# Kernel optimization log

Measured on AMD Instinct MI355X. Metric: run time of the kernel, lower is better.

## Reference

```python
import jax, jax.numpy as jnp
import numpy as np

D_MODEL = 1024
D_FF = 4096
N_EXPERTS = 8
B, S = 4, 2048


def setup_inputs() -> dict:
    key = jax.random.key(0)
    ks = jax.random.split(key, 6)
    x = jax.random.normal(ks[0], (B, S, D_MODEL), dtype=jnp.float32)
    # router: nn.Linear(d_model, num_experts) with bias (default torch init ~ small)
    gate_W = jax.random.normal(ks[1], (N_EXPERTS, D_MODEL), dtype=jnp.float32) * 0.02
    gate_b = jnp.zeros((N_EXPERTS,), dtype=jnp.float32)
    # SwiGLU expert weights, bias-free; torch Linear stores [out, in]
    Wg = jax.random.normal(ks[2], (N_EXPERTS, D_FF, D_MODEL), dtype=jnp.float32) * 0.02
    W1 = jax.random.normal(ks[3], (N_EXPERTS, D_FF, D_MODEL), dtype=jnp.float32) * 0.02
    W2 = jax.random.normal(ks[4], (N_EXPERTS, D_MODEL, D_FF), dtype=jnp.float32) * (0.02 / np.sqrt(2.0))
    return {"x": x, "gate_W": gate_W, "gate_b": gate_b, "Wg": Wg, "W1": W1, "W2": W2,
            "num_experts_per_token": 2}


def reference(x, gate_W, gate_b, Wg, W1, W2, num_experts_per_token):
    """Eval-mode ExpertFeedForward: top-k gating + per-expert SwiGLU + weighted combine."""
    Bb, Ss, D = x.shape
    E = gate_W.shape[0]
    T = Bb * Ss
    xt = x.reshape(T, D)  # [T, D] tokens

    # router logits and top-k softmax over selected experts
    logits = xt @ gate_W.T + gate_b              # [T, E]
    scores, idx = jax.lax.top_k(logits, num_experts_per_token)  # [T, k]
    probs = jax.nn.softmax(scores, axis=-1)      # softmax over top-k only

    # combine weights per (token, expert): scatter top-k probs into dense [T, E]
    tok = jnp.arange(T)[:, None]
    cw = jnp.zeros((T, E), dtype=x.dtype).at[tok, idx].add(probs)  # [T, E]

    out = jnp.zeros_like(xt)
    for e in range(E):  # small fixed expert count
        gate = jax.nn.silu(xt @ Wg[e].T)         # [T, d_ff]
        val = xt @ W1[e].T                       # [T, d_ff]
        y = (gate * val) @ W2[e].T               # [T, D]
        out = out + y * cw[:, e:e + 1]
    return out.reshape(Bb, Ss, D)
```

## Files before the change

kernel.cpp:

```cpp
#include <hip/hip_runtime.h>

#define T_TOKENS 8192
#define D_MODEL  1024
#define D_FF     4096
#define N_EXP    8

#define BM 128
#define BN 128
#define BK 32
#define SP 40

typedef __attribute__((ext_vector_type(8))) short bf16x8;
typedef __attribute__((ext_vector_type(4))) float f32x4;

__device__ __forceinline__ unsigned short f2bf(float f) {
    unsigned int u = __float_as_uint(f);
    u += 0x7fffu + ((u >> 16) & 1u);
    return (unsigned short)(u >> 16);
}

__global__ void router_kernel(const float* __restrict__ x, const float* __restrict__ gW,
                              const float* __restrict__ gb, int* __restrict__ counts,
                              int* __restrict__ top_e, float* __restrict__ top_p) {
    int t    = blockIdx.x * 4 + (threadIdx.x >> 6);
    int lane = threadIdx.x & 63;
    const float* xr = x + (size_t)t * D_MODEL;
    float acc[N_EXP];
#pragma unroll
    for (int e = 0; e < N_EXP; e++) acc[e] = 0.f;
    for (int i = 0; i < D_MODEL / 64; i++) {
        float xv = xr[lane + i * 64];
#pragma unroll
        for (int e = 0; e < N_EXP; e++) acc[e] += xv * gW[e * D_MODEL + lane + i * 64];
    }
#pragma unroll
    for (int e = 0; e < N_EXP; e++) {
#pragma unroll
        for (int off = 32; off > 0; off >>= 1) acc[e] += __shfl_down(acc[e], off, 64);
    }
    if (lane == 0) {
#pragma unroll
        for (int e = 0; e < N_EXP; e++) acc[e] += gb[e];
        int e0 = 0;
#pragma unroll
        for (int e = 1; e < N_EXP; e++) if (acc[e] > acc[e0]) e0 = e;
        int e1 = (e0 == 0) ? 1 : 0;
#pragma unroll
        for (int e = 0; e < N_EXP; e++) if (e != e0 && e != e1 && acc[e] > acc[e1]) e1 = e;
        float z1 = __expf(acc[e1] - acc[e0]);
        float s  = 1.f + z1;
        top_e[t * 2]     = e0;
        top_e[t * 2 + 1] = e1;
        top_p[t * 2]     = 1.f / s;
        top_p[t * 2 + 1] = z1 / s;
        atomicAdd(&counts[e0], 1);
        atomicAdd(&counts[e1], 1);
    }
}

__global__ void prefix_kernel(const int* __restrict__ counts, int* __restrict__ offsets,
                              int* __restrict__ cursor) {
    if (threadIdx.x == 0) {
        int s = 0;
        for (int e = 0; e < N_EXP; e++) { offsets[e] = s; cursor[e] = s; s += counts[e]; }
    }
}

__global__ void scatter_kernel(const int* __restrict__ top_e, const float* __restrict__ top_p,
                               int* __restrict__ cursor, int* __restrict__ row_map,
                               float* __restrict__ row_prob) {
    int t = blockIdx.x * 256 + threadIdx.x;
#pragma unroll
    for (int j = 0; j < 2; j++) {
        int e  = top_e[t * 2 + j];
        int pos = atomicAdd(&cursor[e], 1);
        row_map[pos]  = t;
        row_prob[pos] = top_p[t * 2 + j];
    }
}

__launch_bounds__(256, 2)
__global__ void gemm1_kernel(const float* __restrict__ x, const float* __restrict__ Wg,
                             const float* __restrict__ W1, const int* __restrict__ counts,
                             const int* __restrict__ offsets, const int* __restrict__ row_map,
                             unsigned short* __restrict__ hbuf) {
    int e   = blockIdx.z;
    int cnt = counts[e];
    int m0  = blockIdx.y * BM;
    if (m0 >= cnt) return;
    int base = offsets[e];
    int n0   = blockIdx.x * BN;
    int tid  = threadIdx.x;

    __shared__ unsigned short As[BM * SP];
    __shared__ unsigned short Bg[BN * SP];
    __shared__ unsigned short Bv[BN * SP];
    __shared__ int rowIdx[BM];

    if (tid < BM) {
        int i = m0 + tid;
        if (i > cnt - 1) i = cnt - 1;
        rowIdx[tid] = row_map[base + i];
    }
    __syncthreads();

    const float* wg = Wg + (size_t)e * D_FF * D_MODEL;
    const float* w1 = W1 + (size_t)e * D_FF * D_MODEL;

    int wave = tid >> 6, lane = tid & 63;
    int wm = (wave >> 1) * 64, wn = (wave & 1) * 64;
    int lm = lane & 15, lq = lane >> 4;

    f32x4 accG[4][4], accV[4][4];
#pragma unroll
    for (int i = 0; i < 4; i++)
#pragma unroll
        for (int j = 0; j < 4; j++) { accG[i][j] = (f32x4)0.f; accV[i][j] = (f32x4)0.f; }

    for (int kk = 0; kk < D_MODEL; kk += BK) {
#pragma unroll
        for (int l = 0; l < 4; l++) {
            int idx = tid + l * 256;
            int r = idx >> 3, s = idx & 7;
            float4 v = *(const float4*)(x + (size_t)rowIdx[r] * D_MODEL + kk + s * 4);
            unsigned short* d = &As[r * SP + s * 4];
            d[0] = f2bf(v.x); d[1] = f2bf(v.y); d[2] = f2bf(v.z); d[3] = f2bf(v.w);
        }
#pragma unroll
        for (int l = 0; l < 4; l++) {
            int idx = tid + l * 256;
            int r = idx >> 3, s = idx & 7;
            float4 v = *(const float4*)(wg + (size_t)(n0 + r) * D_MODEL + kk + s * 4);
            unsigned short* d = &Bg[r * SP + s * 4];
            d[0] = f2bf(v.x); d[1] = f2bf(v.y); d[2] = f2bf(v.z); d[3] = f2bf(v.w);
        }
#pragma unroll
        for (int l = 0; l < 4; l++) {
            int idx = tid + l * 256;
            int r = idx >> 3, s = idx & 7;
            float4 v = *(const float4*)(w1 + (size_t)(n0 + r) * D_MODEL + kk + s * 4);
            unsigned short* d = &Bv[r * SP + s * 4];
            d[0] = f2bf(v.x); d[1] = f2bf(v.y); d[2] = f2bf(v.z); d[3] = f2bf(v.w);
        }
        __syncthreads();

        bf16x8 aF[4], bgF[4], bvF[4];
#pragma unroll
        for (int mi = 0; mi < 4; mi++)
            aF[mi] = *(const bf16x8*)&As[(wm + mi * 16 + lm) * SP + lq * 8];
#pragma unroll
        for (int ni = 0; ni < 4; ni++) {
            bgF[ni] = *(const bf16x8*)&Bg[(wn + ni * 16 + lm) * SP + lq * 8];
            bvF[ni] = *(const bf16x8*)&Bv[(wn + ni * 16 + lm) * SP + lq * 8];
        }
#pragma unroll
        for (int mi = 0; mi < 4; mi++)
#pragma unroll
            for (int ni = 0; ni < 4; ni++) {
                accG[mi][ni] = __builtin_amdgcn_mfma_f32_16x16x32_bf16(aF[mi], bgF[ni], accG[mi][ni], 0, 0, 0);
                accV[mi][ni] = __builtin_amdgcn_mfma_f32_16x16x32_bf16(aF[mi], bvF[ni], accV[mi][ni], 0, 0, 0);
            }
        __syncthreads();
    }

    size_t hrow_base = (size_t)(base + m0);
#pragma unroll
    for (int mi = 0; mi < 4; mi++) {
#pragma unroll
        for (int r = 0; r < 4; r++) {
            int mrow = wm + mi * 16 + lq * 4 + r;
            if (m0 + mrow < cnt) {
                unsigned short* hp = hbuf + (hrow_base + mrow) * D_FF + n0 + wn;
#pragma unroll
                for (int ni = 0; ni < 4; ni++) {
                    float g = accG[mi][ni][r], v = accV[mi][ni][r];
                    float sg = g / (1.f + __expf(-g));
                    hp[ni * 16 + lm] = f2bf(sg * v);
                }
            }
        }
    }
}

__launch_bounds__(256, 2)
__global__ void gemm2_kernel(const unsigned short* __restrict__ hbuf, const float* __restrict__ W2,
                             const int* __restrict__ counts, const int* __restrict__ offsets,
                             const int* __restrict__ row_map, const float* __restrict__ row_prob,
                             float* __restrict__ out) {
    int e   = blockIdx.z;
    int cnt = counts[e];
    int m0  = blockIdx.y * BM;
    if (m0 >= cnt) return;
    int base = offsets[e];
    int n0   = blockIdx.x * BN;
    int tid  = threadIdx.x;

    __shared__ unsigned short As[BM * SP];
    __shared__ unsigned short Bs[BN * SP];
    __shared__ int   tok[BM];
    __shared__ float prb[BM];

    if (tid < BM) {
        int i = m0 + tid;
        if (i > cnt - 1) i = cnt - 1;
        tok[tid] = row_map[base + i];
        prb[tid] = row_prob[base + i];
    }
    __syncthreads();

    const float* w2 = W2 + (size_t)e * D_MODEL * D_FF;

    int wave = tid >> 6, lane = tid & 63;
    int wm = (wave >> 1) * 64, wn = (wave & 1) * 64;
    int lm = lane & 15, lq = lane >> 4;

    f32x4 acc[4][4];
#pragma unroll
    for (int i = 0; i < 4; i++)
#pragma unroll
        for (int j = 0; j < 4; j++) acc[i][j] = (f32x4)0.f;

    for (int kk = 0; kk < D_FF; kk += BK) {
#pragma unroll
        for (int l = 0; l < 2; l++) {
            int idx = tid + l * 256;
            int r = idx >> 2, s = idx & 3;
            int rr = m0 + r;
            if (rr > cnt - 1) rr = cnt - 1;
            uint4 v = *(const uint4*)(hbuf + (size_t)(base + rr) * D_FF + kk + s * 8);
            *(uint4*)&As[r * SP + s * 8] = v;
        }
#pragma unroll
        for (int l = 0; l < 4; l++) {
            int idx = tid + l * 256;
            int r = idx >> 3, s = idx & 7;
            float4 v = *(const float4*)(w2 + (size_t)(n0 + r) * D_FF + kk + s * 4);
            unsigned short* d = &Bs[r * SP + s * 4];
            d[0] = f2bf(v.x); d[1] = f2bf(v.y); d[2] = f2bf(v.z); d[3] = f2bf(v.w);
        }
        __syncthreads();

        bf16x8 aF[4], bF[4];
#pragma unroll
        for (int mi = 0; mi < 4; mi++)
            aF[mi] = *(const bf16x8*)&As[(wm + mi * 16 + lm) * SP + lq * 8];
#pragma unroll
        for (int ni = 0; ni < 4; ni++)
            bF[ni] = *(const bf16x8*)&Bs[(wn + ni * 16 + lm) * SP + lq * 8];
#pragma unroll
        for (int mi = 0; mi < 4; mi++)
#pragma unroll
            for (int ni = 0; ni < 4; ni++)
                acc[mi][ni] = __builtin_amdgcn_mfma_f32_16x16x32_bf16(aF[mi], bF[ni], acc[mi][ni], 0, 0, 0);
        __syncthreads();
    }

#pragma unroll
    for (int mi = 0; mi < 4; mi++) {
#pragma unroll
        for (int r = 0; r < 4; r++) {
            int mrow = wm + mi * 16 + lq * 4 + r;
            if (m0 + mrow < cnt) {
                int   t = tok[mrow];
                float p = prb[mrow];
                float* op = out + (size_t)t * D_MODEL + n0 + wn;
#pragma unroll
                for (int ni = 0; ni < 4; ni++)
                    atomicAdd(&op[ni * 16 + lm], p * acc[mi][ni][r]);
            }
        }
    }
}

extern "C" void kernel_launch(void* const* d_in, const int* in_sizes, int n_in,
                              void* d_out, int out_size, void* d_ws, size_t ws_size,
                              hipStream_t stream) {
    const float* x  = (const float*)d_in[0];
    const float* gW = (const float*)d_in[1];
    const float* gb = (const float*)d_in[2];
    const float* Wg = (const float*)d_in[3];
    const float* W1 = (const float*)d_in[4];
    const float* W2 = (const float*)d_in[5];
    float* out = (float*)d_out;

    char* ws = (char*)d_ws;
    int*   counts   = (int*)ws;
    int*   offsets  = (int*)(ws + 64);
    int*   cursor   = (int*)(ws + 128);
    int*   row_map  = (int*)(ws + 256);
    float* row_prob = (float*)(ws + 256 + 65536);
    int*   top_e    = (int*)(ws + 256 + 2 * 65536);
    float* top_p    = (float*)(ws + 256 + 3 * 65536);
    unsigned short* hbuf = (unsigned short*)(ws + 256 + 4 * 65536);

    hipMemsetAsync(ws, 0, 256, stream);
    hipMemsetAsync(d_out, 0, (size_t)T_TOKENS * D_MODEL * sizeof(float), stream);

    router_kernel<<<T_TOKENS / 4, 256, 0, stream>>>(x, gW, gb, counts, top_e, top_p);
    prefix_kernel<<<1, 64, 0, stream>>>(counts, offsets, cursor);
    scatter_kernel<<<T_TOKENS / 256, 256, 0, stream>>>(top_e, top_p, cursor, row_map, row_prob);
    gemm1_kernel<<<dim3(D_FF / BN, T_TOKENS / BM, N_EXP), 256, 0, stream>>>(
        x, Wg, W1, counts, offsets, row_map, hbuf);
    gemm2_kernel<<<dim3(D_MODEL / BN, T_TOKENS / BM, N_EXP), 256, 0, stream>>>(
        hbuf, W2, counts, offsets, row_map, row_prob, out);
}
```

Measured before the change: 1.387 ms.

## Pre-convert weights and gathered activations to bf16 and use direct global-to-LDS loads

Adds kernels that convert the fp32 expert weights and the gathered, per-expert-sorted x rows to bf16 once per call. The GEMMs then read these bf16 buffers with global_load_lds DMA into XOR-swizzled, unpadded shared tiles, so the repeated per-tile fp32-to-bf16 conversion and scattered row indexing disappear from the inner loops. The routing probability is folded into the gemm1 epilogue before the bf16 store, which removes the multiply from gemm2's atomic epilogue. The trade-offs are extra conversion passes over about 400 MB of fp32 weights per call and reuse of the Wg buffer for W2. The main loop still loads a single LDS buffer and synchronises before computing, so loads are not overlapped with MFMA work.

```diff
diff --git a/kernel.cpp b/kernel.cpp
--- a/kernel.cpp
+++ b/kernel.cpp
@@ -8,7 +8,6 @@
 #define BM 128
 #define BN 128
 #define BK 32
-#define SP 40
 
 typedef __attribute__((ext_vector_type(8))) short bf16x8;
 typedef __attribute__((ext_vector_type(4))) float f32x4;
@@ -17,6 +16,22 @@
     unsigned int u = __float_as_uint(f);
     u += 0x7fffu + ((u >> 16) & 1u);
     return (unsigned short)(u >> 16);
+}
+
+__device__ __forceinline__ void gld16(const unsigned short* g, unsigned short* l) {
+    __builtin_amdgcn_global_load_lds(
+        (const __attribute__((address_space(1))) unsigned int*)g,
+        (__attribute__((address_space(3))) unsigned int*)l, 16, 0, 0);
+}
+
+__global__ void cvt_kernel(const float* __restrict__ src, unsigned short* __restrict__ dst) {
+    size_t i = ((size_t)blockIdx.x * 256 + threadIdx.x) * 8;
+    float4 a = *(const float4*)(src + i);
+    float4 b = *(const float4*)(src + i + 4);
+    union { unsigned short u[8]; uint4 v; } r;
+    r.u[0] = f2bf(a.x); r.u[1] = f2bf(a.y); r.u[2] = f2bf(a.z); r.u[3] = f2bf(a.w);
+    r.u[4] = f2bf(b.x); r.u[5] = f2bf(b.y); r.u[6] = f2bf(b.z); r.u[7] = f2bf(b.w);
+    *(uint4*)(dst + i) = r.v;
 }
 
 __global__ void router_kernel(const float* __restrict__ x, const float* __restrict__ gW,
@@ -79,10 +94,26 @@
     }
 }
 
+__global__ void gather_x_kernel(const float* __restrict__ x, const int* __restrict__ row_map,
+                                unsigned short* __restrict__ xg) {
+    int pos = blockIdx.x * 2 + (threadIdx.x >> 7);
+    int c   = (threadIdx.x & 127) * 8;
+    int t   = row_map[pos];
+    float4 a = *(const float4*)(x + (size_t)t * D_MODEL + c);
+    float4 b = *(const float4*)(x + (size_t)t * D_MODEL + c + 4);
+    union { unsigned short u[8]; uint4 v; } r;
+    r.u[0] = f2bf(a.x); r.u[1] = f2bf(a.y); r.u[2] = f2bf(a.z); r.u[3] = f2bf(a.w);
+    r.u[4] = f2bf(b.x); r.u[5] = f2bf(b.y); r.u[6] = f2bf(b.z); r.u[7] = f2bf(b.w);
+    *(uint4*)(xg + (size_t)pos * D_MODEL + c) = r.v;
+}
+
+
 __launch_bounds__(256, 2)
-__global__ void gemm1_kernel(const float* __restrict__ x, const float* __restrict__ Wg,
-                             const float* __restrict__ W1, const int* __restrict__ counts,
-                             const int* __restrict__ offsets, const int* __restrict__ row_map,
+__global__ void gemm1_kernel(const unsigned short* __restrict__ xg,
+                             const unsigned short* __restrict__ wgb,
+                             const unsigned short* __restrict__ w1b,
+                             const int* __restrict__ counts, const int* __restrict__ offsets,
+                             const float* __restrict__ row_prob,
                              unsigned short* __restrict__ hbuf) {
     int e   = blockIdx.z;
     int cnt = counts[e];
@@ -91,25 +122,44 @@
     int base = offsets[e];
     int n0   = blockIdx.x * BN;
     int tid  = threadIdx.x;
-
-    __shared__ unsigned short As[BM * SP];
-    __shared__ unsigned short Bg[BN * SP];
-    __shared__ unsigned short Bv[BN * SP];
-    __shared__ int rowIdx[BM];
+    int wave = tid >> 6, lane = tid & 63;
+
+    __shared__ unsigned short As[BM * BK];
+    __shared__ unsigned short Bg[BN * BK];
+    __shared__ unsigned short Bv[BN * BK];
+    __shared__ float prb[BM];
 
     if (tid < BM) {
-        int i = m0 + tid;
-        if (i > cnt - 1) i = cnt - 1;
-        rowIdx[tid] = row_map[base + i];
-    }
-    __syncthreads();
-
-    const float* wg = Wg + (size_t)e * D_FF * D_MODEL;
-    const float* w1 = W1 + (size_t)e * D_FF * D_MODEL;
-
-    int wave = tid >> 6, lane = tid & 63;
+        int i = m0 + tid; if (i > cnt - 1) i = cnt - 1;
+        prb[tid] = row_prob[base + i];
+    }
+
+    const unsigned short* wg = wgb + (size_t)e * D_FF * D_MODEL;
+    const unsigned short* w1 = w1b + (size_t)e * D_FF * D_MODEL;
+
+    const unsigned short* gA[2]; const unsigned short* gG[2]; const unsigned short* gV[2];
+    unsigned short* lA[2]; unsigned short* lG[2]; unsigned short* lV[2];
+#pragma unroll
+    for (int l = 0; l < 2; l++) {
+        int cell = wave * 64 + l * 256 + lane;
+        int row  = cell >> 2;
+        int kb   = (cell & 3) ^ (row & 3);
+        int ra = m0 + row; if (ra > cnt - 1) ra = cnt - 1;
+        gA[l] = xg + (size_t)(base + ra) * D_MODEL + kb * 8;
+        gG[l] = wg + (size_t)(n0 + row) * D_MODEL + kb * 8;
+        gV[l] = w1 + (size_t)(n0 + row) * D_MODEL + kb * 8;
+        int c0 = wave * 64 + l * 256;
+        lA[l] = As + c0 * 8;
+        lG[l] = Bg + c0 * 8;
+        lV[l] = Bv + c0 * 8;
+    }
+
     int wm = (wave >> 1) * 64, wn = (wave & 1) * 64;
     int lm = lane & 15, lq = lane >> 4;
+    int swz = lq ^ (lm & 3);
+    const bf16x8* aP = (const bf16x8*)(As + ((wm + lm) * 4 + swz) * 8);
+    const bf16x8* gP = (const bf16x8*)(Bg + ((wn + lm) * 4 + swz) * 8);
+    const bf16x8* vP = (const bf16x8*)(Bv + ((wn + lm) * 4 + swz) * 8);
 
     f32x4 accG[4][4], accV[4][4];
 #pragma unroll
@@ -118,41 +168,17 @@
         for (int j = 0; j < 4; j++) { accG[i][j] = (f32x4)0.f; accV[i][j] = (f32x4)0.f; }
 
     for (int kk = 0; kk < D_MODEL; kk += BK) {
-#pragma unroll
-        for (int l = 0; l < 4; l++) {
-            int idx = tid + l * 256;
-            int r = idx >> 3, s = idx & 7;
-            float4 v = *(const float4*)(x + (size_t)rowIdx[r] * D_MODEL + kk + s * 4);
-            unsigned short* d = &As[r * SP + s * 4];
-            d[0] = f2bf(v.x); d[1] = f2bf(v.y); d[2] = f2bf(v.z); d[3] = f2bf(v.w);
-        }
-#pragma unroll
-        for (int l = 0; l < 4; l++) {
-            int idx = tid + l * 256;
-            int r = idx >> 3, s = idx & 7;
-            float4 v = *(const float4*)(wg + (size_t)(n0 + r) * D_MODEL + kk + s * 4);
-            unsigned short* d = &Bg[r * SP + s * 4];
-            d[0] = f2bf(v.x); d[1] = f2bf(v.y); d[2] = f2bf(v.z); d[3] = f2bf(v.w);
-        }
-#pragma unroll
-        for (int l = 0; l < 4; l++) {
-            int idx = tid + l * 256;
-            int r = idx >> 3, s = idx & 7;
-            float4 v = *(const float4*)(w1 + (size_t)(n0 + r) * D_MODEL + kk + s * 4);
-            unsigned short* d = &Bv[r * SP + s * 4];
-            d[0] = f2bf(v.x); d[1] = f2bf(v.y); d[2] = f2bf(v.z); d[3] = f2bf(v.w);
-        }
+        gld16(gA[0], lA[0]); gld16(gA[1], lA[1]);
+        gld16(gG[0], lG[0]); gld16(gG[1], lG[1]);
+        gld16(gV[0], lV[0]); gld16(gV[1], lV[1]);
+        gA[0] += BK; gA[1] += BK; gG[0] += BK; gG[1] += BK; gV[0] += BK; gV[1] += BK;
         __syncthreads();
 
         bf16x8 aF[4], bgF[4], bvF[4];
 #pragma unroll
-        for (int mi = 0; mi < 4; mi++)
-            aF[mi] = *(const bf16x8*)&As[(wm + mi * 16 + lm) * SP + lq * 8];
-#pragma unroll
-        for (int ni = 0; ni < 4; ni++) {
-            bgF[ni] = *(const bf16x8*)&Bg[(wn + ni * 16 + lm) * SP + lq * 8];
-            bvF[ni] = *(const bf16x8*)&Bv[(wn + ni * 16 + lm) * SP + lq * 8];
-        }
+        for (int mi = 0; mi < 4; mi++) aF[mi] = aP[mi * 64];
+#pragma unroll
+        for (int ni = 0; ni < 4; ni++) { bgF[ni] = gP[ni * 64]; bvF[ni] = vP[ni * 64]; }
 #pragma unroll
         for (int mi = 0; mi < 4; mi++)
 #pragma unroll
@@ -170,12 +196,13 @@
         for (int r = 0; r < 4; r++) {
             int mrow = wm + mi * 16 + lq * 4 + r;
             if (m0 + mrow < cnt) {
+                float p = prb[mrow];
                 unsigned short* hp = hbuf + (hrow_base + mrow) * D_FF + n0 + wn;
 #pragma unroll
                 for (int ni = 0; ni < 4; ni++) {
                     float g = accG[mi][ni][r], v = accV[mi][ni][r];
                     float sg = g / (1.f + __expf(-g));
-                    hp[ni * 16 + lm] = f2bf(sg * v);
+                    hp[ni * 16 + lm] = f2bf(sg * v * p);
                 }
             }
         }
@@ -183,9 +210,10 @@
 }
 
 __launch_bounds__(256, 2)
-__global__ void gemm2_kernel(const unsigned short* __restrict__ hbuf, const float* __restrict__ W2,
+__global__ void gemm2_kernel(const unsigned short* __restrict__ hbuf,
+                             const unsigned short* __restrict__ w2b,
                              const int* __restrict__ counts, const int* __restrict__ offsets,
-                             const int* __restrict__ row_map, const float* __restrict__ row_prob,
+                             const int* __restrict__ row_map,
                              float* __restrict__ out) {
     int e   = blockIdx.z;
     int cnt = counts[e];
@@ -194,25 +222,39 @@
     int base = offsets[e];
     int n0   = blockIdx.x * BN;
     int tid  = threadIdx.x;
-
-    __shared__ unsigned short As[BM * SP];
-    __shared__ unsigned short Bs[BN * SP];
-    __shared__ int   tok[BM];
-    __shared__ float prb[BM];
+    int wave = tid >> 6, lane = tid & 63;
+
+    __shared__ unsigned short As[BM * BK];
+    __shared__ unsigned short Bs[BN * BK];
+    __shared__ int tok[BM];
 
     if (tid < BM) {
-        int i = m0 + tid;
-        if (i > cnt - 1) i = cnt - 1;
+        int i = m0 + tid; if (i > cnt - 1) i = cnt - 1;
         tok[tid] = row_map[base + i];
-        prb[tid] = row_prob[base + i];
-    }
-    __syncthreads();
-
-    const float* w2 = W2 + (size_t)e * D_MODEL * D_FF;
-
-    int wave = tid >> 6, lane = tid & 63;
+    }
+
+    const unsigned short* w2 = w2b + (size_t)e * D_MODEL * D_FF;
+
+    const unsigned short* gA[2]; const unsigned short* gB[2];
+    unsigned short* lA[2]; unsigned short* lB[2];
+#pragma unroll
+    for (int l = 0; l < 2; l++) {
+        int cell = wave * 64 + l * 256 + lane;
+        int row  = cell >> 2;
+        int kb   = (cell & 3) ^ (row & 3);
+        int ra = m0 + row; if (ra > cnt - 1) ra = cnt - 1;
+        gA[l] = hbuf + (size_t)(base + ra) * D_FF + kb * 8;
+        gB[l] = w2 + (size_t)(n0 + row) * D_FF + kb * 8;
+        int c0 = wave * 64 + l * 256;
+        lA[l] = As + c0 * 8;
+        lB[l] = Bs + c0 * 8;
+    }
+
     int wm = (wave >> 1) * 64, wn = (wave & 1) * 64;
     int lm = lane & 15, lq = lane >> 4;
+    int swz = lq ^ (lm & 3);
+    const bf16x8* aP = (const bf16x8*)(As + ((wm + lm) * 4 + swz) * 8);
+    const bf16x8* bP = (const bf16x8*)(Bs + ((wn + lm) * 4 + swz) * 8);
 
     f32x4 acc[4][4];
 #pragma unroll
@@ -221,32 +263,16 @@
         for (int j = 0; j < 4; j++) acc[i][j] = (f32x4)0.f;
 
     for (int kk = 0; kk < D_FF; kk += BK) {
-#pragma unroll
-        for (int l = 0; l < 2; l++) {
-            int idx = tid + l * 256;
-            int r = idx >> 2, s = idx & 3;
-            int rr = m0 + r;
-            if (rr > cnt - 1) rr = cnt - 1;
-            uint4 v = *(const uint4*)(hbuf + (size_t)(base + rr) * D_FF + kk + s * 8);
-            *(uint4*)&As[r * SP + s * 8] = v;
-        }
-#pragma unroll
-        for (int l = 0; l < 4; l++) {
-            int idx = tid + l * 256;
-            int r = idx >> 3, s = idx & 7;
-            float4 v = *(const float4*)(w2 + (size_t)(n0 + r) * D_FF + kk + s * 4);
-            unsigned short* d = &Bs[r * SP + s * 4];
-            d[0] = f2bf(v.x); d[1] = f2bf(v.y); d[2] = f2bf(v.z); d[3] = f2bf(v.w);
-        }
+        gld16(gA[0], lA[0]); gld16(gA[1], lA[1]);
+        gld16(gB[0], lB[0]); gld16(gB[1], lB[1]);
+        gA[0] += BK; gA[1] += BK; gB[0] += BK; gB[1] += BK;
         __syncthreads();
 
         bf16x8 aF[4], bF[4];
 #pragma unroll
-        for (int mi = 0; mi < 4; mi++)
-            aF[mi] = *(const bf16x8*)&As[(wm + mi * 16 + lm) * SP + lq * 8];
-#pragma unroll
-        for (int ni = 0; ni < 4; ni++)
-            bF[ni] = *(const bf16x8*)&Bs[(wn + ni * 16 + lm) * SP + lq * 8];
+        for (int mi = 0; mi < 4; mi++) aF[mi] = aP[mi * 64];
+#pragma unroll
+        for (int ni = 0; ni < 4; ni++) bF[ni] = bP[ni * 64];
 #pragma unroll
         for (int mi = 0; mi < 4; mi++)
 #pragma unroll
@@ -261,12 +287,11 @@
         for (int r = 0; r < 4; r++) {
             int mrow = wm + mi * 16 + lq * 4 + r;
             if (m0 + mrow < cnt) {
-                int   t = tok[mrow];
-                float p = prb[mrow];
+                int t = tok[mrow];
                 float* op = out + (size_t)t * D_MODEL + n0 + wn;
 #pragma unroll
                 for (int ni = 0; ni < 4; ni++)
-                    atomicAdd(&op[ni * 16 + lm], p * acc[mi][ni][r]);
+                    atomicAdd(&op[ni * 16 + lm], acc[mi][ni][r]);
             }
         }
     }
@@ -284,6 +309,7 @@
     float* out = (float*)d_out;
 
     char* ws = (char*)d_ws;
+    const size_t MiB = 1024 * 1024;
     int*   counts   = (int*)ws;
     int*   offsets  = (int*)(ws + 64);
     int*   cursor   = (int*)(ws + 128);
@@ -291,16 +317,24 @@
     float* row_prob = (float*)(ws + 256 + 65536);
     int*   top_e    = (int*)(ws + 256 + 2 * 65536);
     float* top_p    = (float*)(ws + 256 + 3 * 65536);
-    unsigned short* hbuf = (unsigned short*)(ws + 256 + 4 * 65536);
+    unsigned short* wgb  = (unsigned short*)(ws + 1 * MiB);
+    unsigned short* w1b  = (unsigned short*)(ws + 65 * MiB);
+    unsigned short* xg   = (unsigned short*)(ws + 129 * MiB);
+    unsigned short* hbuf = (unsigned short*)(ws + 161 * MiB);
+    unsigned short* w2b  = wgb;
 
     hipMemsetAsync(ws, 0, 256, stream);
     hipMemsetAsync(d_out, 0, (size_t)T_TOKENS * D_MODEL * sizeof(float), stream);
 
+    cvt_kernel<<<16384, 256, 0, stream>>>(Wg, wgb);
+    cvt_kernel<<<16384, 256, 0, stream>>>(W1, w1b);
     router_kernel<<<T_TOKENS / 4, 256, 0, stream>>>(x, gW, gb, counts, top_e, top_p);
     prefix_kernel<<<1, 64, 0, stream>>>(counts, offsets, cursor);
     scatter_kernel<<<T_TOKENS / 256, 256, 0, stream>>>(top_e, top_p, cursor, row_map, row_prob);
+    gather_x_kernel<<<T_TOKENS, 256, 0, stream>>>(x, row_map, xg);
     gemm1_kernel<<<dim3(D_FF / BN, T_TOKENS / BM, N_EXP), 256, 0, stream>>>(
-        x, Wg, W1, counts, offsets, row_map, hbuf);
+        xg, wgb, w1b, counts, offsets, row_prob, hbuf);
+    cvt_kernel<<<16384, 256, 0, stream>>>(W2, w2b);
     gemm2_kernel<<<dim3(D_MODEL / BN, T_TOKENS / BM, N_EXP), 256, 0, stream>>>(
-        hbuf, W2, counts, offsets, row_map, row_prob, out);
-}
+        hbuf, w2b, counts, offsets, row_map, out);
+}
```

Measured after the change: 1.300 ms. 1.07x faster.
